# Kernel optimization log

Measured on AMD Instinct MI355X. Metric: run time of the kernel, lower is better.

Reference implementation:

```python
import jax, jax.numpy as jnp
import numpy as np

B, S, E, H, L = 4, 512, 768, 12, 12
D = E // H
FF = 4 * E
EPS = 1e-5
SCALE = jnp.float32(768.0 ** 0.5)  # emb_size ** (1/2), applied AFTER softmax per source


def setup_inputs() -> dict:
    key = jax.random.key(0)
    ks = jax.random.split(key, 18)
    std = 0.02
    n = lambda k, shp: (jax.random.normal(k, shp, jnp.float32) * std)
    return {
        "x": jax.random.normal(ks[0], (B, S, E), jnp.float32),
        "Wqkv": n(ks[1], (L, E, 3 * E)),
        "bqkv": n(ks[2], (L, 3 * E)),
        "Wp": n(ks[3], (L, E, E)),
        "bp": n(ks[4], (L, E)),
        "W1": n(ks[5], (L, E, FF)),
        "b1": n(ks[6], (L, FF)),
        "W2": n(ks[7], (L, FF, E)),
        "b2": n(ks[8], (L, E)),
        "ln1_g": jnp.ones((L, E), jnp.float32), "ln1_b": jnp.zeros((L, E), jnp.float32),
        "ln2_g": jnp.ones((L, E), jnp.float32), "ln2_b": jnp.zeros((L, E), jnp.float32),
        "ln3_g": jnp.ones((L, E), jnp.float32), "ln3_b": jnp.zeros((L, E), jnp.float32),
        "ln4_g": jnp.ones((L, E), jnp.float32), "ln4_b": jnp.zeros((L, E), jnp.float32),
    }


def _ln(x, g, b):
    m = jnp.mean(x, axis=-1, keepdims=True)
    v = jnp.mean(jnp.square(x - m), axis=-1, keepdims=True)
    return (x - m) * jax.lax.rsqrt(v + EPS) * g + b


def _block(x, p):
    Wqkv, bqkv, Wp, bp, W1, b1, W2, b2, g1, be1, g2, be2, g3, be3, g4, be4 = p
    # --- attention branch ---
    h = _ln(x, g1, be1)
    qkv = h @ Wqkv + bqkv                      # [B,S,3E]
    qkv = qkv.reshape(B, S, H, D, 3)           # qkv is innermost factor in source rearrange
    q = jnp.transpose(qkv[..., 0], (0, 2, 1, 3))  # [B,H,S,D]
    k = jnp.transpose(qkv[..., 1], (0, 2, 1, 3))
    v = jnp.transpose(qkv[..., 2], (0, 2, 1, 3))
    energy = jnp.einsum('bhqd,bhkd->bhqk', q, k)
    att = jax.nn.softmax(energy, axis=-1) / SCALE  # NOTE: scaling AFTER softmax (faithful)
    o = jnp.einsum('bhqk,bhkd->bhqd', att, v)
    o = jnp.transpose(o, (0, 2, 1, 3)).reshape(B, S, E)
    o = o @ Wp + bp
    r1 = _ln(o, g2, be2) + x                   # first ResidualAdd (final LN inside branch)
    # --- feed-forward branch ---
    f = _ln(r1, g3, be3)
    f = jax.nn.gelu(f @ W1 + b1, approximate=False)
    f = f @ W2 + b2
    r2 = _ln(f, g4, be4) + r1                  # second ResidualAdd
    return x + r2                              # outer residual: x = x + block(x)


def reference(x, Wqkv, bqkv, Wp, bp, W1, b1, W2, b2,
              ln1_g, ln1_b, ln2_g, ln2_b, ln3_g, ln3_b, ln4_g, ln4_b):
    params = (Wqkv, bqkv, Wp, bp, W1, b1, W2, b2,
              ln1_g, ln1_b, ln2_g, ln2_b, ln3_g, ln3_b, ln4_g, ln4_b)
    out, _ = jax.lax.scan(lambda c, p: (_block(c, p), None), x, params)
    return out
```

## Files before the change

### kernel.cpp

```cpp
#include <hip/hip_runtime.h>
#include <hip/hip_bf16.h>
#include <stdint.h>

#define LAYERS 12
#define M_ROWS 2048
#define E_DIM 768
#define FF_DIM 3072
#define QKV_DIM 2304
#define SCALE_INV 0.036084391824351615f

typedef __hip_bfloat16 bf16;
typedef __attribute__((ext_vector_type(8))) __bf16 bf16x8;
typedef __attribute__((ext_vector_type(4))) float f32x4;

__device__ __forceinline__ float bf2f(bf16 v) { return __bfloat162float(v); }
__device__ __forceinline__ bf16 f2bf(float v) { return __float2bfloat16(v); }

__device__ __forceinline__ float gelu_f(float x) {
  return 0.5f * x * (1.0f + erff(x * 0.70710678118654752f));
}

__device__ __forceinline__ void async16(const bf16* g, bf16* l) {
  __builtin_amdgcn_global_load_lds(
      (const __attribute__((address_space(1))) void*)g,
      (__attribute__((address_space(3))) void*)l, 16, 0, 0);
}

__global__ __launch_bounds__(256) void transpose_all_k(
    const float* __restrict__ Wqkv, const float* __restrict__ Wp,
    const float* __restrict__ W1, const float* __restrict__ W2,
    bf16* __restrict__ tq, bf16* __restrict__ tp,
    bf16* __restrict__ t1, bf16* __restrict__ t2)
{
  __shared__ float T[32][33];
  int l = blockIdx.y;
  int bid = blockIdx.x;
  const float* src; bf16* dst; int K, N, tile;
  if (bid < 1728)      { src = Wqkv + (size_t)l * 768 * 2304; dst = tq + (size_t)l * 768 * 2304; K = 768;  N = 2304; tile = bid; }
  else if (bid < 2304) { src = Wp   + (size_t)l * 768 * 768;  dst = tp + (size_t)l * 768 * 768;  K = 768;  N = 768;  tile = bid - 1728; }
  else if (bid < 4608) { src = W1   + (size_t)l * 768 * 3072; dst = t1 + (size_t)l * 768 * 3072; K = 768;  N = 3072; tile = bid - 2304; }
  else                 { src = W2   + (size_t)l * 3072 * 768; dst = t2 + (size_t)l * 3072 * 768; K = 3072; N = 768;  tile = bid - 4608; }
  int tilesN = N >> 5;
  int tk = tile / tilesN;
  int tn = tile - tk * tilesN;
  int tx = threadIdx.x & 31, ty = threadIdx.x >> 5;
  int k0 = tk << 5, n0 = tn << 5;
#pragma unroll
  for (int i = 0; i < 4; i++)
    T[ty + i * 8][tx] = src[(size_t)(k0 + ty + i * 8) * N + n0 + tx];
  __syncthreads();
#pragma unroll
  for (int i = 0; i < 4; i++)
    dst[(size_t)(n0 + ty + i * 8) * K + k0 + tx] = f2bf(T[tx][ty + i * 8]);
}

template<int OUT_BF16, int NADD, int NPART>
__global__ __launch_bounds__(256) void ln_k(
    const float* __restrict__ in, const float* __restrict__ gamma,
    const float* __restrict__ beta, const float* __restrict__ add0,
    const float* __restrict__ add1, void* __restrict__ outp)
{
  int row = blockIdx.x, tid = threadIdx.x;
  size_t rb = (size_t)row * 768;
  float v[3]; float s = 0.f, sq = 0.f;
#pragma unroll
  for (int j = 0; j < 3; j++) {
    int c = tid + j * 256;
    float x = in[rb + c];
    if (NPART == 2) x += in[(size_t)M_ROWS * 768 + rb + c];
    v[j] = x;
    s += x; sq += x * x;
  }
#pragma unroll
  for (int off = 32; off; off >>= 1) {
    s += __shfl_xor(s, off);
    sq += __shfl_xor(sq, off);
  }
  __shared__ float red[8];
  int wv = tid >> 6;
  if ((tid & 63) == 0) { red[wv] = s; red[4 + wv] = sq; }
  __syncthreads();
  s  = red[0] + red[1] + red[2] + red[3];
  sq = red[4] + red[5] + red[6] + red[7];
  float mean = s * (1.0f / 768.0f);
  float var  = sq * (1.0f / 768.0f) - mean * mean;
  float rstd = rsqrtf(var + 1e-5f);
#pragma unroll
  for (int j = 0; j < 3; j++) {
    int c = tid + j * 256;
    float val = (v[j] - mean) * rstd * gamma[c] + beta[c];
    if (NADD >= 1) val += add0[rb + c];
    if (NADD >= 2) val += add1[rb + c];
    if (OUT_BF16) ((bf16*)outp)[rb + c] = f2bf(val);
    else          ((float*)outp)[rb + c] = val;
  }
}

template<int NADD, int NPART, int WRITE2>
__global__ __launch_bounds__(256) void lnln_k(
    const float* __restrict__ in, const float* __restrict__ gA,
    const float* __restrict__ bA, const float* __restrict__ add0,
    const float* __restrict__ add1, float* __restrict__ out1,
    const float* __restrict__ gB, const float* __restrict__ bB,
    bf16* __restrict__ out2)
{
  int row = blockIdx.x, tid = threadIdx.x;
  size_t rb = (size_t)row * 768;
  __shared__ float red[8];
  int wv = tid >> 6;

  float v[3]; float s = 0.f, sq = 0.f;
#pragma unroll
  for (int j = 0; j < 3; j++) {
    int c = tid + j * 256;
    float x = in[rb + c];
    if (NPART == 2) x += in[(size_t)M_ROWS * 768 + rb + c];
    v[j] = x;
    s += x; sq += x * x;
  }
#pragma unroll
  for (int off = 32; off; off >>= 1) {
    s += __shfl_xor(s, off);
    sq += __shfl_xor(sq, off);
  }
  if ((tid & 63) == 0) { red[wv] = s; red[4 + wv] = sq; }
  __syncthreads();
  s  = red[0] + red[1] + red[2] + red[3];
  sq = red[4] + red[5] + red[6] + red[7];
  float mean = s * (1.0f / 768.0f);
  float var  = sq * (1.0f / 768.0f) - mean * mean;
  float rstd = rsqrtf(var + 1e-5f);

  float y[3]; float s2 = 0.f, sq2 = 0.f;
#pragma unroll
  for (int j = 0; j < 3; j++) {
    int c = tid + j * 256;
    float t = (v[j] - mean) * rstd * gA[c] + bA[c];
    if (NADD >= 1) t += add0[rb + c];
    if (NADD >= 2) t += add1[rb + c];
    y[j] = t;
    out1[rb + c] = t;
    s2 += t; sq2 += t * t;
  }
  if (WRITE2) {
#pragma unroll
    for (int off = 32; off; off >>= 1) {
      s2 += __shfl_xor(s2, off);
      sq2 += __shfl_xor(sq2, off);
    }
    __syncthreads();
    if ((tid & 63) == 0) { red[wv] = s2; red[4 + wv] = sq2; }
    __syncthreads();
    s2  = red[0] + red[1] + red[2] + red[3];
    sq2 = red[4] + red[5] + red[6] + red[7];
    float mean2 = s2 * (1.0f / 768.0f);
    float var2  = sq2 * (1.0f / 768.0f) - mean2 * mean2;
    float rstd2 = rsqrtf(var2 + 1e-5f);
#pragma unroll
    for (int j = 0; j < 3; j++) {
      int c = tid + j * 256;
      out2[rb + c] = f2bf((y[j] - mean2) * rstd2 * gB[c] + bB[c]);
    }
  }
}

template<int OUT_MODE, int NSPLIT>
__global__ __launch_bounds__(256) void gemm2_k(
    const bf16* __restrict__ A, const bf16* __restrict__ BT,
    const float* __restrict__ bias, void* __restrict__ Cout,
    bf16* __restrict__ qo, bf16* __restrict__ ko, bf16* __restrict__ vo,
    int N, int K)
{
  __shared__ __align__(16) bf16 Als[2][128 * 32];
  __shared__ __align__(16) bf16 Bls[2][64 * 32];
  int tid = threadIdx.x;
  int lane = tid & 63, w = tid >> 6;
  int l15 = lane & 15, l4 = lane >> 4;
  int Nt = N >> 6;
  int mt = blockIdx.x / Nt, ntile = blockIdx.x - mt * Nt;
  int m0 = mt << 7, n0 = ntile << 6;
  int sp = (NSPLIT > 1) ? blockIdx.y : 0;
  int Kc = K / NSPLIT;
  int kbeg = sp * Kc, kend = kbeg + Kc;
  const bf16* Ap = A + (size_t)m0 * K;
  const bf16* Bp = BT + (size_t)n0 * K;
  int ar = tid >> 2;
  int ac = (tid & 3) * 8;

  f32x4 acc[2][4] = {};

  async16(Ap + (size_t)ar * K + kbeg + ac,        &Als[0][w * 512]);
  async16(Ap + (size_t)(ar + 64) * K + kbeg + ac, &Als[0][2048 + w * 512]);
  async16(Bp + (size_t)ar * K + kbeg + ac,        &Bls[0][w * 512]);
  __syncthreads();

  int cur = 0;
  for (int k0 = kbeg; k0 < kend; k0 += 32) {
    if (k0 + 32 < kend) {
      int kn = k0 + 32;
      async16(Ap + (size_t)ar * K + kn + ac,        &Als[cur ^ 1][w * 512]);
      async16(Ap + (size_t)(ar + 64) * K + kn + ac, &Als[cur ^ 1][2048 + w * 512]);
      async16(Bp + (size_t)ar * K + kn + ac,        &Bls[cur ^ 1][w * 512]);
    }
    bf16x8 af[2], bfr[4];
#pragma unroll
    for (int i = 0; i < 2; i++)
      af[i] = *(const bf16x8*)&Als[cur][(w * 32 + i * 16 + l15) * 32 + l4 * 8];
#pragma unroll
    for (int j = 0; j < 4; j++)
      bfr[j] = *(const bf16x8*)&Bls[cur][(j * 16 + l15) * 32 + l4 * 8];
#pragma unroll
    for (int i = 0; i < 2; i++)
#pragma unroll
      for (int j = 0; j < 4; j++)
        acc[i][j] = __builtin_amdgcn_mfma_f32_16x16x32_bf16(af[i], bfr[j], acc[i][j], 0, 0, 0);
    __syncthreads();
    cur ^= 1;
  }

#pragma unroll
  for (int i = 0; i < 2; i++) {
    int mbase = m0 + w * 32 + i * 16 + (l4 << 2);
#pragma unroll
    for (int j = 0; j < 4; j++) {
      int n = n0 + j * 16 + l15;
      float bvs = (NSPLIT == 1 || sp == 0) ? bias[n] : 0.0f;
      if (OUT_MODE == 3) {
        int h = n / 192;
        int rm = n - h * 192;
        int d = rm / 3;
        int t = rm - d * 3;
#pragma unroll
        for (int rg = 0; rg < 4; rg++) {
          int m = mbase + rg;
          float val = acc[i][j][rg] + bvs;
          int b = m >> 9, sIdx = m & 511;
          int bh = b * 12 + h;
          if (t == 2)
            vo[(size_t)((bh << 6) + d) * 512 + sIdx] = f2bf(val);
          else {
            bf16* dsts = (t == 0) ? qo : ko;
            dsts[(size_t)((bh << 9) + sIdx) * 64 + d] = f2bf(val);
          }
        }
      } else {
#pragma unroll
        for (int rg = 0; rg < 4; rg++) {
          int m = mbase + rg;
          float val = acc[i][j][rg] + bvs;
          if (OUT_MODE == 0)
            ((float*)Cout)[(size_t)sp * M_ROWS * N + (size_t)m * N + n] = val;
          else if (OUT_MODE == 1)
            ((bf16*)Cout)[(size_t)m * N + n] = f2bf(val);
          else
            ((bf16*)Cout)[(size_t)m * N + n] = f2bf(gelu_f(val));
        }
      }
    }
  }
}

#define PSTR 80
__global__ __launch_bounds__(256) void attn_k(
    const bf16* __restrict__ q, const bf16* __restrict__ k,
    const bf16* __restrict__ vT, bf16* __restrict__ o)
{
  __shared__ __align__(16) bf16 Kls[64 * 64];
  __shared__ __align__(16) bf16 Vls[64 * 64];
  __shared__ __align__(16) bf16 Pls[4][16 * PSTR];
  int tid = threadIdx.x;
  int lane = tid & 63, w = tid >> 6;
  int l15 = lane & 15, l4 = lane >> 4;
  int qt = blockIdx.x & 7;
  int bh = blockIdx.x >> 3;
  size_t base = (size_t)bh * 32768;

  const bf16* qrowp = q + base + (size_t)(qt * 64 + w * 16 + l15) * 64 + l4 * 8;
  bf16x8 qf0 = *(const bf16x8*)qrowp;
  bf16x8 qf1 = *(const bf16x8*)(qrowp + 32);

  int rr = tid >> 3, cc = (tid & 7) * 8;
  const bf16* ksrc = k + base + (size_t)rr * 64 + cc;
  const bf16* vsrc = vT + base + (size_t)rr * 512 + cc;

  float mrow[4] = {-1e30f, -1e30f, -1e30f, -1e30f};
  float lsum[4] = {0.f, 0.f, 0.f, 0.f};
  f32x4 Oacc[4] = {};
  const f32x4 zed = {0.f, 0.f, 0.f, 0.f};
  bf16* pw = &Pls[w][0];

  for (int kt = 0; kt < 8; kt++) {
    __syncthreads();
    async16(ksrc + (size_t)kt * 4096,        &Kls[w * 512]);
    async16(ksrc + (size_t)kt * 4096 + 2048, &Kls[2048 + w * 512]);
    async16(vsrc + kt * 64,                  &Vls[w * 512]);
    async16(vsrc + kt * 64 + (size_t)32 * 512, &Vls[2048 + w * 512]);
    __syncthreads();
    f32x4 e[4];
#pragma unroll
    for (int jt = 0; jt < 4; jt++) {
      bf16x8 kf0 = *(const bf16x8*)&Kls[(jt * 16 + l15) * 64 + l4 * 8];
      bf16x8 kf1 = *(const bf16x8*)&Kls[(jt * 16 + l15) * 64 + l4 * 8 + 32];
      e[jt] = __builtin_amdgcn_mfma_f32_16x16x32_bf16(qf0, kf0, zed, 0, 0, 0);
      e[jt] = __builtin_amdgcn_mfma_f32_16x16x32_bf16(qf1, kf1, e[jt], 0, 0, 0);
    }
    float al[4];
#pragma unroll
    for (int rg = 0; rg < 4; rg++) {
      float mn = fmaxf(fmaxf(e[0][rg], e[1][rg]), fmaxf(e[2][rg], e[3][rg]));
#pragma unroll
      for (int off = 1; off < 16; off <<= 1) mn = fmaxf(mn, __shfl_xor(mn, off));
      float mnew = fmaxf(mrow[rg], mn);
      al[rg] = __expf(mrow[rg] - mnew);
      mrow[rg] = mnew;
    }
    float rs[4] = {0.f, 0.f, 0.f, 0.f};
#pragma unroll
    for (int jt = 0; jt < 4; jt++)
#pragma unroll
      for (int rg = 0; rg < 4; rg++) {
        float p = __expf(e[jt][rg] - mrow[rg]);
        rs[rg] += p;
        pw[(l4 * 4 + rg) * PSTR + jt * 16 + l15] = f2bf(p);
      }
#pragma unroll
    for (int rg = 0; rg < 4; rg++) {
#pragma unroll
      for (int off = 1; off < 16; off <<= 1) rs[rg] += __shfl_xor(rs[rg], off);
      lsum[rg] = lsum[rg] * al[rg] + rs[rg];
    }
#pragma unroll
    for (int dt = 0; dt < 4; dt++)
#pragma unroll
      for (int rg = 0; rg < 4; rg++) Oacc[dt][rg] *= al[rg];
    bf16x8 pf0 = *(const bf16x8*)&pw[l15 * PSTR + l4 * 8];
    bf16x8 pf1 = *(const bf16x8*)&pw[l15 * PSTR + l4 * 8 + 32];
#pragma unroll
    for (int dt = 0; dt < 4; dt++) {
      bf16x8 vf0 = *(const bf16x8*)&Vls[(dt * 16 + l15) * 64 + l4 * 8];
      bf16x8 vf1 = *(const bf16x8*)&Vls[(dt * 16 + l15) * 64 + l4 * 8 + 32];
      Oacc[dt] = __builtin_amdgcn_mfma_f32_16x16x32_bf16(pf0, vf0, Oacc[dt], 0, 0, 0);
      Oacc[dt] = __builtin_amdgcn_mfma_f32_16x16x32_bf16(pf1, vf1, Oacc[dt], 0, 0, 0);
    }
  }
  int b = bh / 12, h = bh - b * 12;
#pragma unroll
  for (int rg = 0; rg < 4; rg++) {
    int qrow = qt * 64 + w * 16 + l4 * 4 + rg;
    float inv = SCALE_INV / lsum[rg];
    size_t rowoff = (size_t)(b * 512 + qrow) * 768 + h * 64;
#pragma unroll
    for (int dt = 0; dt < 4; dt++)
      o[rowoff + dt * 16 + l15] = f2bf(Oacc[dt][rg] * inv);
  }
}

extern "C" void kernel_launch(void* const* d_in, const int* in_sizes, int n_in,
                              void* d_out, int out_size, void* d_ws, size_t ws_size,
                              hipStream_t stream)
{
  const float* x    = (const float*)d_in[0];
  const float* Wqkv = (const float*)d_in[1];
  const float* bqkv = (const float*)d_in[2];
  const float* Wp   = (const float*)d_in[3];
  const float* bp   = (const float*)d_in[4];
  const float* W1   = (const float*)d_in[5];
  const float* b1   = (const float*)d_in[6];
  const float* W2   = (const float*)d_in[7];
  const float* b2   = (const float*)d_in[8];
  const float* g1  = (const float*)d_in[9];
  const float* be1 = (const float*)d_in[10];
  const float* g2  = (const float*)d_in[11];
  const float* be2 = (const float*)d_in[12];
  const float* g3  = (const float*)d_in[13];
  const float* be3 = (const float*)d_in[14];
  const float* g4  = (const float*)d_in[15];
  const float* be4 = (const float*)d_in[16];
  float* xout = (float*)d_out;

  char* ws = (char*)d_ws;
  size_t off = 0;
  auto alloc = [&](size_t bytes) -> char* {
    char* p = ws + off;
    off += (bytes + 255) & ~(size_t)255;
    return p;
  };
  const size_t NTOK = (size_t)M_ROWS * E_DIM;
  bf16*  qb  = (bf16*)alloc(NTOK * 2);
  bf16*  kb  = (bf16*)alloc(NTOK * 2);
  bf16*  vb  = (bf16*)alloc(NTOK * 2);
  bf16*  hb  = (bf16*)alloc(NTOK * 2);
  bf16*  ob  = (bf16*)alloc(NTOK * 2);
  bf16*  f1b = (bf16*)alloc((size_t)M_ROWS * FF_DIM * 2);
  float* tmp = (float*)alloc(NTOK * 4 * 2);
  float* r1  = (float*)alloc(NTOK * 4);
  bf16*  tq  = (bf16*)alloc((size_t)LAYERS * 768 * 2304 * 2);
  bf16*  tp  = (bf16*)alloc((size_t)LAYERS * 768 * 768 * 2);
  bf16*  t1  = (bf16*)alloc((size_t)LAYERS * 768 * 3072 * 2);
  bf16*  t2  = (bf16*)alloc((size_t)LAYERS * 3072 * 768 * 2);
  if (off > ws_size) {
    hipMemsetAsync(d_out, 0x7f, (size_t)out_size * 4, stream);
    return;
  }

  transpose_all_k<<<dim3(6912, LAYERS), 256, 0, stream>>>(
      Wqkv, Wp, W1, W2, tq, tp, t1, t2);

  hipMemcpyAsync(d_out, x, (size_t)out_size * 4, hipMemcpyDeviceToDevice, stream);

  ln_k<1, 0, 1><<<2048, 256, 0, stream>>>(xout, g1, be1, nullptr, nullptr, hb);

  for (int l = 0; l < LAYERS; l++) {
    const bf16* tq_l = tq + (size_t)l * 768 * 2304;
    const bf16* tp_l = tp + (size_t)l * 768 * 768;
    const bf16* t1_l = t1 + (size_t)l * 768 * 3072;
    const bf16* t2_l = t2 + (size_t)l * 3072 * 768;

    gemm2_k<3, 1><<<dim3(16 * 36, 1), 256, 0, stream>>>(
        hb, tq_l, bqkv + (size_t)l * 2304, nullptr, qb, kb, vb, 2304, 768);
    attn_k<<<384, 256, 0, stream>>>(qb, kb, vb, ob);
    gemm2_k<0, 2><<<dim3(16 * 12, 2), 256, 0, stream>>>(
        ob, tp_l, bp + (size_t)l * 768, tmp, nullptr, nullptr, nullptr, 768, 768);
    lnln_k<1, 2, 1><<<2048, 256, 0, stream>>>(
        tmp, g2 + l * 768, be2 + l * 768, xout, nullptr, r1,
        g3 + l * 768, be3 + l * 768, hb);
    gemm2_k<2, 1><<<dim3(16 * 48, 1), 256, 0, stream>>>(
        hb, t1_l, b1 + (size_t)l * 3072, f1b, nullptr, nullptr, nullptr, 3072, 768);
    gemm2_k<0, 2><<<dim3(16 * 12, 2), 256, 0, stream>>>(
        f1b, t2_l, b2 + (size_t)l * 768, tmp, nullptr, nullptr, nullptr, 768, 3072);
    if (l + 1 < LAYERS) {
      lnln_k<2, 2, 1><<<2048, 256, 0, stream>>>(
          tmp, g4 + l * 768, be4 + l * 768, r1, xout, xout,
          g1 + (l + 1) * 768, be1 + (l + 1) * 768, hb);
    } else {
      lnln_k<2, 2, 0><<<2048, 256, 0, stream>>>(
          tmp, g4 + l * 768, be4 + l * 768, r1, xout, xout,
          nullptr, nullptr, nullptr);
    }
  }
}
```

Baseline: 1.990 ms.

## Use 2-wave GEMM blocks with 64x64 per-wave tiles; vectorize and permute weight transpose

The GEMM now launches 128 threads (2 waves), each computing a 64x64 output sub-tile. That raises per-wave register reuse of A/B fragments and issues 16 MFMAs per k-step instead of 8, at the cost of fewer waves per block for latency hiding. The weight transpose uses 64x64 tiles with float4 loads and 16-byte bf16 stores. It also permutes the QKV weight columns so the epilogue's q/k/v index math becomes cheap shifts, with the bias index remapped to match. The transpose runs once per call, so its cost stays inside the timed region.

```diff
diff --git a/kernel.cpp b/kernel.cpp
--- a/kernel.cpp
+++ b/kernel.cpp
@@ -32,26 +32,45 @@
     bf16* __restrict__ tq, bf16* __restrict__ tp,
     bf16* __restrict__ t1, bf16* __restrict__ t2)
 {
-  __shared__ float T[32][33];
+  __shared__ float T[64][65];
   int l = blockIdx.y;
   int bid = blockIdx.x;
-  const float* src; bf16* dst; int K, N, tile;
-  if (bid < 1728)      { src = Wqkv + (size_t)l * 768 * 2304; dst = tq + (size_t)l * 768 * 2304; K = 768;  N = 2304; tile = bid; }
-  else if (bid < 2304) { src = Wp   + (size_t)l * 768 * 768;  dst = tp + (size_t)l * 768 * 768;  K = 768;  N = 768;  tile = bid - 1728; }
-  else if (bid < 4608) { src = W1   + (size_t)l * 768 * 3072; dst = t1 + (size_t)l * 768 * 3072; K = 768;  N = 3072; tile = bid - 2304; }
-  else                 { src = W2   + (size_t)l * 3072 * 768; dst = t2 + (size_t)l * 3072 * 768; K = 3072; N = 768;  tile = bid - 4608; }
-  int tilesN = N >> 5;
-  int tk = tile / tilesN;
-  int tn = tile - tk * tilesN;
-  int tx = threadIdx.x & 31, ty = threadIdx.x >> 5;
-  int k0 = tk << 5, n0 = tn << 5;
-#pragma unroll
-  for (int i = 0; i < 4; i++)
-    T[ty + i * 8][tx] = src[(size_t)(k0 + ty + i * 8) * N + n0 + tx];
+  const float* src; bf16* dst; int K, N, tile, perm;
+  if (bid < 432)       { src = Wqkv + (size_t)l * 768 * 2304; dst = tq + (size_t)l * 768 * 2304; K = 768;  N = 2304; tile = bid;        perm = 1; }
+  else if (bid < 576)  { src = Wp   + (size_t)l * 768 * 768;  dst = tp + (size_t)l * 768 * 768;  K = 768;  N = 768;  tile = bid - 432;  perm = 0; }
+  else if (bid < 1152) { src = W1   + (size_t)l * 768 * 3072; dst = t1 + (size_t)l * 768 * 3072; K = 768;  N = 3072; tile = bid - 576;  perm = 0; }
+  else                 { src = W2   + (size_t)l * 3072 * 768; dst = t2 + (size_t)l * 3072 * 768; K = 3072; N = 768;  tile = bid - 1152; perm = 0; }
+  int tilesN = N >> 6;
+  int tk = tile / tilesN, tn = tile - tk * tilesN;
+  int k0 = tk << 6, n0 = tn << 6;
+  int t = threadIdx.x;
+  int lrow = t >> 4, lcol = (t & 15) * 4;
+#pragma unroll
+  for (int it = 0; it < 4; it++) {
+    int row = it * 16 + lrow;
+    const float4 v4 = *(const float4*)&src[(size_t)(k0 + row) * N + n0 + lcol];
+    T[row][lcol] = v4.x; T[row][lcol + 1] = v4.y;
+    T[row][lcol + 2] = v4.z; T[row][lcol + 3] = v4.w;
+  }
   __syncthreads();
-#pragma unroll
-  for (int i = 0; i < 4; i++)
-    dst[(size_t)(n0 + ty + i * 8) * K + k0 + tx] = f2bf(T[tx][ty + i * 8]);
+  int kc = (t & 7) * 8, nb = t >> 3;
+#pragma unroll
+  for (int it = 0; it < 2; it++) {
+    int nrow = it * 32 + nb;
+    int n = n0 + nrow;
+    int ncol = n;
+    if (perm) {
+      int h = n / 192;
+      int rm = n - h * 192;
+      int d = rm / 3;
+      int t3 = rm - d * 3;
+      ncol = t3 * 768 + h * 64 + d;
+    }
+    union { bf16 h8[8]; uint4 v; } u;
+#pragma unroll
+    for (int j = 0; j < 8; j++) u.h8[j] = f2bf(T[kc + j][nrow]);
+    *(uint4*)&dst[(size_t)ncol * K + k0 + kc] = u.v;
+  }
 }
 
 template<int OUT_BF16, int NADD, int NPART>
@@ -165,7 +184,7 @@
 }
 
 template<int OUT_MODE, int NSPLIT>
-__global__ __launch_bounds__(256) void gemm2_k(
+__global__ __launch_bounds__(128) void gemm5_k(
     const bf16* __restrict__ A, const bf16* __restrict__ BT,
     const float* __restrict__ bias, void* __restrict__ Cout,
     bf16* __restrict__ qo, bf16* __restrict__ ko, bf16* __restrict__ vo,
@@ -181,55 +200,63 @@
   int m0 = mt << 7, n0 = ntile << 6;
   int sp = (NSPLIT > 1) ? blockIdx.y : 0;
   int Kc = K / NSPLIT;
-  int kbeg = sp * Kc, kend = kbeg + Kc;
-  const bf16* Ap = A + (size_t)m0 * K;
-  const bf16* Bp = BT + (size_t)n0 * K;
-  int ar = tid >> 2;
-  int ac = (tid & 3) * 8;
-
-  f32x4 acc[2][4] = {};
-
-  async16(Ap + (size_t)ar * K + kbeg + ac,        &Als[0][w * 512]);
-  async16(Ap + (size_t)(ar + 64) * K + kbeg + ac, &Als[0][2048 + w * 512]);
-  async16(Bp + (size_t)ar * K + kbeg + ac,        &Bls[0][w * 512]);
+  int kbeg = sp * Kc;
+  int nsteps = Kc >> 5;
+  int sr = tid >> 2;
+  int sc = (tid & 3) * 8;
+  const bf16* a_src = A + (size_t)(m0 + sr) * K + kbeg + sc;
+  const bf16* b_src = BT + (size_t)(n0 + sr) * K + kbeg + sc;
+
+  f32x4 acc[4][4] = {};
+
+#define STAGE5(buf)                                                  \
+  do {                                                               \
+    async16(a_src,                   &Als[buf][w * 512]);            \
+    async16(a_src + (size_t)32 * K,  &Als[buf][1024 + w * 512]);     \
+    async16(a_src + (size_t)64 * K,  &Als[buf][2048 + w * 512]);     \
+    async16(a_src + (size_t)96 * K,  &Als[buf][3072 + w * 512]);     \
+    async16(b_src,                   &Bls[buf][w * 512]);            \
+    async16(b_src + (size_t)32 * K,  &Bls[buf][1024 + w * 512]);     \
+  } while (0)
+
+  STAGE5(0);
   __syncthreads();
 
   int cur = 0;
-  for (int k0 = kbeg; k0 < kend; k0 += 32) {
-    if (k0 + 32 < kend) {
-      int kn = k0 + 32;
-      async16(Ap + (size_t)ar * K + kn + ac,        &Als[cur ^ 1][w * 512]);
-      async16(Ap + (size_t)(ar + 64) * K + kn + ac, &Als[cur ^ 1][2048 + w * 512]);
-      async16(Bp + (size_t)ar * K + kn + ac,        &Bls[cur ^ 1][w * 512]);
-    }
-    bf16x8 af[2], bfr[4];
-#pragma unroll
-    for (int i = 0; i < 2; i++)
-      af[i] = *(const bf16x8*)&Als[cur][(w * 32 + i * 16 + l15) * 32 + l4 * 8];
+  for (int ks = 0; ks < nsteps; ks++) {
+    if (ks + 1 < nsteps) {
+      a_src += 32; b_src += 32;
+      STAGE5(cur ^ 1);
+    }
+    bf16x8 af[4], bfr[4];
+#pragma unroll
+    for (int i = 0; i < 4; i++)
+      af[i] = *(const bf16x8*)&Als[cur][(w * 64 + i * 16 + l15) * 32 + l4 * 8];
 #pragma unroll
     for (int j = 0; j < 4; j++)
       bfr[j] = *(const bf16x8*)&Bls[cur][(j * 16 + l15) * 32 + l4 * 8];
 #pragma unroll
-    for (int i = 0; i < 2; i++)
+    for (int i = 0; i < 4; i++)
 #pragma unroll
       for (int j = 0; j < 4; j++)
         acc[i][j] = __builtin_amdgcn_mfma_f32_16x16x32_bf16(af[i], bfr[j], acc[i][j], 0, 0, 0);
     __syncthreads();
     cur ^= 1;
   }
-
-#pragma unroll
-  for (int i = 0; i < 2; i++) {
-    int mbase = m0 + w * 32 + i * 16 + (l4 << 2);
+#undef STAGE5
+
+#pragma unroll
+  for (int i = 0; i < 4; i++) {
+    int mbase = m0 + w * 64 + i * 16 + (l4 << 2);
 #pragma unroll
     for (int j = 0; j < 4; j++) {
       int n = n0 + j * 16 + l15;
-      float bvs = (NSPLIT == 1 || sp == 0) ? bias[n] : 0.0f;
       if (OUT_MODE == 3) {
-        int h = n / 192;
-        int rm = n - h * 192;
-        int d = rm / 3;
-        int t = rm - d * 3;
+        int t = (n >= 1536) ? 2 : (n >= 768 ? 1 : 0);
+        int rm = n - t * 768;
+        int h = rm >> 6;
+        int d = rm & 63;
+        float bvs = bias[h * 192 + d * 3 + t];
 #pragma unroll
         for (int rg = 0; rg < 4; rg++) {
           int m = mbase + rg;
@@ -244,6 +271,7 @@
           }
         }
       } else {
+        float bvs = (NSPLIT == 1 || sp == 0) ? bias[n] : 0.0f;
 #pragma unroll
         for (int rg = 0; rg < 4; rg++) {
           int m = mbase + rg;
@@ -291,9 +319,9 @@
 
   for (int kt = 0; kt < 8; kt++) {
     __syncthreads();
-    async16(ksrc + (size_t)kt * 4096,        &Kls[w * 512]);
-    async16(ksrc + (size_t)kt * 4096 + 2048, &Kls[2048 + w * 512]);
-    async16(vsrc + kt * 64,                  &Vls[w * 512]);
+    async16(ksrc + (size_t)kt * 4096,          &Kls[w * 512]);
+    async16(ksrc + (size_t)kt * 4096 + 2048,   &Kls[2048 + w * 512]);
+    async16(vsrc + kt * 64,                    &Vls[w * 512]);
     async16(vsrc + kt * 64 + (size_t)32 * 512, &Vls[2048 + w * 512]);
     __syncthreads();
     f32x4 e[4];
@@ -403,7 +431,7 @@
     return;
   }
 
-  transpose_all_k<<<dim3(6912, LAYERS), 256, 0, stream>>>(
+  transpose_all_k<<<dim3(1728, LAYERS), 256, 0, stream>>>(
       Wqkv, Wp, W1, W2, tq, tp, t1, t2);
 
   hipMemcpyAsync(d_out, x, (size_t)out_size * 4, hipMemcpyDeviceToDevice, stream);
@@ -416,17 +444,17 @@
     const bf16* t1_l = t1 + (size_t)l * 768 * 3072;
     const bf16* t2_l = t2 + (size_t)l * 3072 * 768;
 
-    gemm2_k<3, 1><<<dim3(16 * 36, 1), 256, 0, stream>>>(
+    gemm5_k<3, 1><<<dim3(16 * 36, 1), 128, 0, stream>>>(
         hb, tq_l, bqkv + (size_t)l * 2304, nullptr, qb, kb, vb, 2304, 768);
     attn_k<<<384, 256, 0, stream>>>(qb, kb, vb, ob);
-    gemm2_k<0, 2><<<dim3(16 * 12, 2), 256, 0, stream>>>(
+    gemm5_k<0, 2><<<dim3(16 * 12, 2), 128, 0, stream>>>(
         ob, tp_l, bp + (size_t)l * 768, tmp, nullptr, nullptr, nullptr, 768, 768);
     lnln_k<1, 2, 1><<<2048, 256, 0, stream>>>(
         tmp, g2 + l * 768, be2 + l * 768, xout, nullptr, r1,
         g3 + l * 768, be3 + l * 768, hb);
-    gemm2_k<2, 1><<<dim3(16 * 48, 1), 256, 0, stream>>>(
+    gemm5_k<2, 1><<<dim3(16 * 48, 1), 128, 0, stream>>>(
         hb, t1_l, b1 + (size_t)l * 3072, f1b, nullptr, nullptr, nullptr, 3072, 768);
-    gemm2_k<0, 2><<<dim3(16 * 12, 2), 256, 0, stream>>>(
+    gemm5_k<0, 2><<<dim3(16 * 12, 2), 128, 0, stream>>>(
         f1b, t2_l, b2 + (size_t)l * 768, tmp, nullptr, nullptr, nullptr, 768, 3072);
     if (l + 1 < LAYERS) {
       lnln_k<2, 2, 1><<<2048, 256, 0, stream>>>(
```

Result: slower. 2.164 ms (+8.8%).
